# Kernel optimization log

Measured on AMD Instinct MI355X. Metric: run time of the kernel, lower is better.

The kernel has to match this reference:

```python
import math
import jax, jax.numpy as jnp
import numpy as np

B, S, D, H = 2, 2048, 2048, 16
HD = D // H
EPS = 1e-6


def _precompute_freqs_cis(dim, end, theta=500000.0):
    inv_freqs = 1.0 / theta ** (np.arange(0, dim, 2, dtype=np.float32) / dim)
    t = np.arange(end, dtype=np.float32)
    freqs = np.outer(t, inv_freqs).astype(np.float32)
    # [1, end, 1, dim//2, 2] matching torch stack(cos, sin, dim=4)
    return jnp.asarray(np.stack([np.cos(freqs)[None, :, None, :], np.sin(freqs)[None, :, None, :]], axis=4))


def setup_inputs() -> dict:
    key = jax.random.key(0)
    k1, k2, k3 = jax.random.split(key, 3)
    x = jax.random.normal(k1, (B, S, D), dtype=jnp.float32)
    w_qkv = jax.random.normal(k2, (3 * D, D), dtype=jnp.float32) * 0.02
    w_out = jax.random.normal(k3, (D, D), dtype=jnp.float32) * 0.02
    attn_scale = jnp.asarray(math.log2(S * S - S), dtype=jnp.float32)
    freqs_cis = _precompute_freqs_cis(HD, S)
    return {"x": x, "w_qkv": w_qkv, "w_out": w_out, "attn_scale": attn_scale, "freqs_cis": freqs_cis}


def _apply_rotary(q, k, fc):
    # q, k: [b, s, h, hd]; fc: [1, s, 1, hd//2, 2]
    b, s, h, hd = q.shape
    qk = jnp.concatenate([q, k], axis=2).reshape(b, s, 2 * h, hd // 2, 2)
    real = qk[..., 0] * fc[..., 0] - qk[..., 1] * fc[..., 1]
    imag = qk[..., 1] * fc[..., 0] + qk[..., 0] * fc[..., 1]
    rot = jnp.stack([real, imag], axis=-1).reshape(b, s, 2 * h, hd)
    return rot[:, :, :h], rot[:, :, h:]


def reference(x, w_qkv, w_out, attn_scale, freqs_cis):
    b, s, d = x.shape
    qkv = x @ w_qkv.T                      # [b, s, 3d]
    q, k, v = jnp.split(qkv, 3, axis=2)
    q = q.reshape(b, s, H, HD)
    k = k.reshape(b, s, H, HD)
    v = v.reshape(b, s, H, HD)
    q, k = _apply_rotary(q, k, freqs_cis[:, :s])
    # -> [b, h, s, hd]
    q = q.transpose(0, 2, 1, 3)
    k = k.transpose(0, 2, 1, 3)
    v = v.transpose(0, 2, 1, 3)
    # per-head L2 norm of q/k, learned scale on q
    q = q / (jnp.linalg.norm(q, axis=-1, keepdims=True) + EPS)
    k = k / (jnp.linalg.norm(k, axis=-1, keepdims=True) + EPS)
    q = q * attn_scale
    # causal SDPA with scale=1.0
    scores = jnp.einsum('bhqd,bhkd->bhqk', q, k)
    causal = jnp.tril(jnp.ones((s, s), dtype=bool))
    scores = jnp.where(causal, scores, -jnp.inf)
    attn = jax.nn.softmax(scores, axis=-1)
    out = jnp.einsum('bhqk,bhkd->bhqd', attn, v)
    out = out.transpose(0, 2, 1, 3).reshape(b, s, d)
    return out @ w_out.T
```

## Files before the change

### kernel.cpp

```cpp
#include <hip/hip_runtime.h>
#include <stdint.h>

#define B_  2
#define S_  2048
#define D_  2048
#define H_  16
#define HD_ 128
#define D3_ 6144

typedef unsigned short u16;
typedef __attribute__((ext_vector_type(8))) __bf16 bf16x8;
typedef __attribute__((ext_vector_type(4))) float f32x4;
typedef __attribute__((ext_vector_type(8))) u16  u16x8;
typedef __attribute__((ext_vector_type(4))) u16  u16x4;
typedef __attribute__((ext_vector_type(2))) u16  u16x2;

__device__ inline u16 f2bf(float f) {
  union { float f; uint32_t u; } v; v.f = f;
  uint32_t r = v.u + 0x7FFFu + ((v.u >> 16) & 1u);
  return (u16)(r >> 16);
}
__device__ inline float bf2f(u16 u) {
  union { float f; uint32_t u; } v; v.u = ((uint32_t)u) << 16;
  return v.f;
}
__device__ inline void gload_lds16(const void* g, void* l) {
  __builtin_amdgcn_global_load_lds((const __attribute__((address_space(1))) uint32_t*)g,
                                   (__attribute__((address_space(3))) uint32_t*)l, 16, 0, 0);
}

#define TILE_SYNC() do { \
    asm volatile("s_waitcnt lgkmcnt(0)" ::: "memory"); \
    asm volatile("s_waitcnt vmcnt(0)" ::: "memory"); \
    __builtin_amdgcn_s_barrier(); \
    asm volatile("" ::: "memory"); \
  } while (0)

__global__ __launch_bounds__(256) void castk3(const float* __restrict__ x, const float* __restrict__ wq,
                                              const float* __restrict__ wo,
                                              u16* __restrict__ xo, u16* __restrict__ wqo, u16* __restrict__ woo) {
  int blk = (int)blockIdx.x;
  const float* in; u16* out; int base;
  if (blk < 4096)       { in = x;  out = xo;  base = blk; }
  else if (blk < 10240) { in = wq; out = wqo; base = blk - 4096; }
  else                  { in = wo; out = woo; base = blk - 10240; }
  int i = base * 256 + (int)threadIdx.x;
  f32x4 a = ((const f32x4*)in)[2*i];
  f32x4 b = ((const f32x4*)in)[2*i + 1];
  u16x8 o;
#pragma unroll
  for (int j = 0; j < 4; ++j) o[j] = f2bf(a[j]);
#pragma unroll
  for (int j = 0; j < 4; ++j) o[4+j] = f2bf(b[j]);
  ((u16x8*)out)[i] = o;
}

template<int BF16OUT>
__global__ __launch_bounds__(512, 2) void gemm384(const u16* __restrict__ A, const u16* __restrict__ Bw,
                                                  void* __restrict__ Cp, int M, int N, int K) {
  __shared__ __align__(16) u16 lds_[40960];
  char* ldsb = (char*)lds_;
  const int tid = threadIdx.x;
  const int w = tid >> 6, l = tid & 63;
  const int lr = l & 15, lg = l >> 4;
  const int wr = w >> 2, wc = w & 3;
  const int nbn = (int)gridDim.x;
  const int nwg = nbn * (int)gridDim.y;
  const int bid = (int)(blockIdx.y * gridDim.x + blockIdx.x);
  const int swz = (bid & 7) * (nwg >> 3) + (bid >> 3);
  const int bm = swz / nbn, bn = swz % nbn;

  f32x4 acc[8][6] = {};

  int mA[2], kA[2], mB[3], kB[3];
#pragma unroll
  for (int p = 0; p < 2; ++p) {
    int off = p*8192 + tid*16; mA[p] = off >> 6;
    kA[p] = (off & 63) ^ (((mA[p] >> 1) & 3) << 4);
  }
#pragma unroll
  for (int p = 0; p < 3; ++p) {
    int off = p*8192 + tid*16; mB[p] = off >> 6;
    kB[p] = (off & 63) ^ (((mB[p] >> 1) & 3) << 4);
  }
  const size_t rs = (size_t)K * 2;
  const char* Ab = (const char*)A + (size_t)bm * 256 * rs;
  const char* Bb = (const char*)Bw + (size_t)bn * 384 * rs;
  const int wb = w * 1024;

#define STG(T_) do { \
    char* dA_ = ldsb + ((T_)&1)*16384; \
    char* dB_ = ldsb + 32768 + ((T_)&1)*24576; \
    _Pragma("unroll") \
    for (int p_ = 0; p_ < 2; ++p_) \
      gload_lds16(Ab + (size_t)mA[p_]*rs + (size_t)(T_)*64 + kA[p_], dA_ + p_*8192 + wb); \
    _Pragma("unroll") \
    for (int p_ = 0; p_ < 3; ++p_) \
      gload_lds16(Bb + (size_t)mB[p_]*rs + (size_t)(T_)*64 + kB[p_], dB_ + p_*8192 + wb); \
  } while (0)

  const int NT = K >> 5;
  STG(0);
  TILE_SYNC();

  for (int T = 0; T < NT; ++T) {
    const char* La = ldsb + (T & 1)*16384;
    const char* Lb = ldsb + 32768 + (T & 1)*24576;
    if (T + 1 < NT) STG(T + 1);

    bf16x8 bfr[6];
#pragma unroll
    for (int nf = 0; nf < 6; ++nf) {
      int row = wc*96 + nf*16 + lr;
      bfr[nf] = *(const bf16x8*)(Lb + row*64 + ((lg*16) ^ (((row >> 1) & 3) << 4)));
    }
#pragma unroll
    for (int mf = 0; mf < 8; ++mf) {
      int row = wr*128 + mf*16 + lr;
      bf16x8 af = *(const bf16x8*)(La + row*64 + ((lg*16) ^ (((row >> 1) & 3) << 4)));
#pragma unroll
      for (int nf = 0; nf < 6; ++nf)
        acc[mf][nf] = __builtin_amdgcn_mfma_f32_16x16x32_bf16(af, bfr[nf], acc[mf][nf], 0, 0, 0);
    }
    TILE_SYNC();
  }
#undef STG

#pragma unroll
  for (int mf = 0; mf < 8; ++mf)
#pragma unroll
    for (int nf = 0; nf < 6; ++nf)
#pragma unroll
      for (int j = 0; j < 4; ++j) {
        int m = bm*256 + wr*128 + mf*16 + lg*4 + j;
        int n = bn*384 + wc*96 + nf*16 + lr;
        float v = acc[mf][nf][j];
        if (BF16OUT) ((u16*)Cp)[(size_t)m * N + n] = f2bf(v);
        else         ((float*)Cp)[(size_t)m * N + n] = v;
      }
}

template<int BF16OUT>
__global__ __launch_bounds__(256, 2) void gemm_bt(const u16* __restrict__ A, const u16* __restrict__ Bw,
                                                  void* __restrict__ Cp, int M, int N, int K) {
  __shared__ __align__(16) u16 lds_[32768];
  char* ldsb = (char*)lds_;
  const int tid = threadIdx.x;
  const int w = tid >> 6, l = tid & 63;
  const int lr = l & 15, lg = l >> 4;
  const int nwg = (int)(gridDim.x * gridDim.y);
  const int bid = (int)(blockIdx.y * gridDim.x + blockIdx.x);
  const int swz = (bid & 7) * (nwg >> 3) + (bid >> 3);
  const int bm = swz / (int)gridDim.x, bn = swz % (int)gridDim.x;
  const int wr = w >> 1, wc = w & 1;

  f32x4 acc[4][4] = {};

  int row4[4], col4[4];
#pragma unroll
  for (int i = 0; i < 4; ++i) {
    int off = i*4096 + tid*16;
    row4[i] = off >> 7;
    col4[i] = (off & 127) ^ ((row4[i] & 7) << 4);
  }
  const size_t rs = (size_t)K * 2;
  const char* Ab = (const char*)A + (size_t)bm * 128 * rs;
  const char* Bb = (const char*)Bw + (size_t)bn * 128 * rs;
  const int wb = w * 1024;

#define STG(T_) do { \
    char* dA_ = ldsb + ((T_)&1)*16384; \
    char* dB_ = ldsb + 32768 + ((T_)&1)*16384; \
    _Pragma("unroll") \
    for (int i_ = 0; i_ < 4; ++i_) \
      gload_lds16(Ab + (size_t)row4[i_]*rs + (size_t)(T_)*128 + col4[i_], dA_ + i_*4096 + wb); \
    _Pragma("unroll") \
    for (int i_ = 0; i_ < 4; ++i_) \
      gload_lds16(Bb + (size_t)row4[i_]*rs + (size_t)(T_)*128 + col4[i_], dB_ + i_*4096 + wb); \
  } while (0)

  const int NT = K >> 6;
  STG(0);
  TILE_SYNC();

  for (int T = 0; T < NT; ++T) {
    const char* La = ldsb + (T & 1)*16384;
    const char* Lb = ldsb + 32768 + (T & 1)*16384;
    if (T + 1 < NT) STG(T + 1);

    bf16x8 af[4][2], bf[4][2];
#pragma unroll
    for (int mt = 0; mt < 4; ++mt) {
      int row = wr*64 + mt*16 + lr;
#pragma unroll
      for (int ks = 0; ks < 2; ++ks)
        af[mt][ks] = *(const bf16x8*)(La + row*128 + ((ks*64 + lg*16) ^ ((row & 7) << 4)));
    }
#pragma unroll
    for (int nt = 0; nt < 4; ++nt) {
      int row = wc*64 + nt*16 + lr;
#pragma unroll
      for (int ks = 0; ks < 2; ++ks)
        bf[nt][ks] = *(const bf16x8*)(Lb + row*128 + ((ks*64 + lg*16) ^ ((row & 7) << 4)));
    }
#pragma unroll
    for (int mt = 0; mt < 4; ++mt)
#pragma unroll
      for (int nt = 0; nt < 4; ++nt) {
        acc[mt][nt] = __builtin_amdgcn_mfma_f32_16x16x32_bf16(af[mt][0], bf[nt][0], acc[mt][nt], 0, 0, 0);
        acc[mt][nt] = __builtin_amdgcn_mfma_f32_16x16x32_bf16(af[mt][1], bf[nt][1], acc[mt][nt], 0, 0, 0);
      }
    TILE_SYNC();
  }
#undef STG

#pragma unroll
  for (int mt = 0; mt < 4; ++mt)
#pragma unroll
    for (int nt = 0; nt < 4; ++nt)
#pragma unroll
      for (int j = 0; j < 4; ++j) {
        int m = bm*128 + wr*64 + mt*16 + lg*4 + j;
        int n = bn*128 + wc*64 + nt*16 + lr;
        float v = acc[mt][nt][j];
        if (BF16OUT) ((u16*)Cp)[(size_t)m * N + n] = f2bf(v);
        else         ((float*)Cp)[(size_t)m * N + n] = v;
      }
}

__global__ __launch_bounds__(256) void rope_norm(const u16* __restrict__ qkv, const float* __restrict__ fc,
                                                 const float* __restrict__ scale_p,
                                                 u16* __restrict__ Qo, u16* __restrict__ Ko) {
  int gid = blockIdx.x;
  int bs = gid >> 2;
  int s = bs & (S_ - 1);
  int b = bs >> 11;
  int w = threadIdx.x >> 6, l = threadIdx.x & 63;
  int h = (gid & 3)*4 + w;
  float2 cs = ((const float2*)fc)[(size_t)s*64 + l];
  float scale = scale_p[0] * 1.4426950408889634f;
  const u16* base = qkv + (size_t)bs * D3_;
  size_t obase = ((size_t)(b*H_ + h) * S_ + s) * HD_ + 2*l;
  {
    const u16* p = base + h*HD_ + 2*l;
    float x0 = bf2f(p[0]), x1 = bf2f(p[1]);
    float r0 = x0*cs.x - x1*cs.y;
    float r1 = x1*cs.x + x0*cs.y;
    float t = r0*r0 + r1*r1;
#pragma unroll
    for (int mk = 1; mk < 64; mk <<= 1) t += __shfl_xor(t, mk, 64);
    float inv = scale / (sqrtf(t) + 1e-6f);
    u16x2 o; o[0] = f2bf(r0*inv); o[1] = f2bf(r1*inv);
    *(u16x2*)(Qo + obase) = o;
  }
  {
    const u16* p = base + D_ + h*HD_ + 2*l;
    float x0 = bf2f(p[0]), x1 = bf2f(p[1]);
    float r0 = x0*cs.x - x1*cs.y;
    float r1 = x1*cs.x + x0*cs.y;
    float t = r0*r0 + r1*r1;
#pragma unroll
    for (int mk = 1; mk < 64; mk <<= 1) t += __shfl_xor(t, mk, 64);
    float inv = 1.0f / (sqrtf(t) + 1e-6f);
    u16x2 o; o[0] = f2bf(r0*inv); o[1] = f2bf(r1*inv);
    *(u16x2*)(Ko + obase) = o;
  }
}

__global__ __launch_bounds__(256) void v_trans(const u16* __restrict__ qkv, u16* __restrict__ Vt) {
  __shared__ u16 vt[64][136];
  int blk = blockIdx.x;
  int bh = blk >> 5, st = blk & 31;
  int b = bh >> 4, h = bh & 15;
  int s0 = st * 64;
  int tid = threadIdx.x;
#pragma unroll
  for (int i = 0; i < 4; ++i) {
    int idx = tid + i*256;
    int row = idx >> 4, ch = idx & 15;
    u16x8 v = *(const u16x8*)(qkv + (size_t)(b*S_ + s0 + row) * D3_ + 2*D_ + h*HD_ + ch*8);
    *(u16x8*)(&vt[row][ch*8]) = v;
  }
  __syncthreads();
#pragma unroll
  for (int p = 0; p < 2; ++p) {
    int d = p*64 + (tid >> 2);
    int q = (tid & 3) * 16;
    u16x8 t0, t1;
#pragma unroll
    for (int i = 0; i < 8; ++i) t0[i] = vt[q + i][d];
#pragma unroll
    for (int i = 0; i < 8; ++i) t1[i] = vt[q + 8 + i][d];
    u16* dst = Vt + ((size_t)bh * HD_ + d) * S_ + s0 + q;
    *(u16x8*)dst = t0;
    *(u16x8*)(dst + 8) = t1;
  }
}

__global__ __launch_bounds__(512) void flash_attn(const u16* __restrict__ Qh, const u16* __restrict__ Kh,
                                                  const u16* __restrict__ Vt, u16* __restrict__ AO) {
  __shared__ __align__(16) u16 lK[2][64*128];
  __shared__ __align__(16) u16 lV[128*64];
  __shared__ __align__(16) u16 lP[8][16*72];
  const int i0 = (int)blockIdx.x;
  const int k5 = i0 & 255;
  const int bh = k5 >> 3;
  const int jj = k5 & 7;
  const int qt = (i0 < 256) ? (15 - jj) : jj;
  const int tid = threadIdx.x, w = tid >> 6, l = tid & 63;
  const int lr = l & 15, lg = l >> 4;
  const int b = bh >> 4, h = bh & 15;

  bf16x8 qf[4];
  {
    const u16* qp = Qh + ((size_t)bh * S_ + qt*128 + w*16 + lr) * HD_ + lg*8;
#pragma unroll
    for (int ks = 0; ks < 4; ++ks) qf[ks] = *(const bf16x8*)(qp + ks*32);
  }
  float m0 = -__builtin_inff(), ls0 = 0.f;
  f32x4 oacc[8] = {};

  int krow[2], kcol[2], vrow[2], vcol[2], dstb[2];
#pragma unroll
  for (int p = 0; p < 2; ++p) {
    int off = p*8192 + tid*16;
    krow[p] = off >> 8; kcol[p] = (off & 255) ^ ((krow[p] & 7) << 4);
    vrow[p] = off >> 7; vcol[p] = (off & 127) ^ ((vrow[p] & 7) << 4);
    dstb[p] = p*8192 + w*1024;
  }
  const char* Kb = (const char*)(Kh + (size_t)bh * S_ * HD_);
  const char* Vb = (const char*)(Vt + (size_t)bh * HD_ * S_);

#define STAGE_K(nb, kt_) do {                                                       \
    _Pragma("unroll")                                                               \
    for (int p_ = 0; p_ < 2; ++p_)                                                  \
      gload_lds16(Kb + (size_t)((kt_)*64 + krow[p_])*256 + kcol[p_],                \
                  (char*)lK[nb] + dstb[p_]);                                        \
  } while (0)
#define STAGE_V(kt_) do {                                                           \
    _Pragma("unroll")                                                               \
    for (int p_ = 0; p_ < 2; ++p_)                                                  \
      gload_lds16(Vb + (size_t)vrow[p_]*(S_*2) + (kt_)*128 + vcol[p_],              \
                  (char*)lV + dstb[p_]);                                            \
  } while (0)

  const int nt = 2*qt + 2;
  STAGE_K(0, 0);
  STAGE_V(0);
  int cur = 0;
  for (int kt = 0; kt < nt; ++kt) {
    asm volatile("s_waitcnt vmcnt(2)" ::: "memory");
    __builtin_amdgcn_s_barrier();
    asm volatile("" ::: "memory");
    const char* lKb = (const char*)lK[cur];

    f32x4 sc[4] = {};
    __builtin_amdgcn_s_setprio(1);
#pragma unroll
    for (int ks = 0; ks < 4; ++ks) {
#pragma unroll
      for (int f = 0; f < 4; ++f) {
        int row = f*16 + lr;
        bf16x8 kf = *(const bf16x8*)(lKb + row*256 + ((ks*64 + lg*16) ^ ((row & 7) << 4)));
        sc[f] = __builtin_amdgcn_mfma_f32_16x16x32_bf16(kf, qf[ks], sc[f], 0, 0, 0);
      }
    }
    __builtin_amdgcn_s_setprio(0);
    if (kt < nt-1) STAGE_K(cur ^ 1, kt + 1);

    if (kt >= nt-2) {
#pragma unroll
      for (int f = 0; f < 4; ++f)
#pragma unroll
        for (int j = 0; j < 4; ++j)
          if (kt*64 + f*16 + lg*4 + j > qt*128 + w*16 + lr) sc[f][j] = -__builtin_inff();
    }
    float pmax = sc[0][0];
#pragma unroll
    for (int f = 0; f < 4; ++f)
#pragma unroll
      for (int j = 0; j < 4; ++j) pmax = fmaxf(pmax, sc[f][j]);
    pmax = fmaxf(pmax, __shfl_xor(pmax, 16, 64));
    pmax = fmaxf(pmax, __shfl_xor(pmax, 32, 64));
    const int norescale = __all(pmax - m0 <= 8.0f);
    float mn;
    float resc = 0.f;
    if (norescale) {
      mn = m0;
    } else {
      mn = fmaxf(m0, pmax);
      resc = exp2f(m0 - mn);
      m0 = mn;
    }
    float rsum = 0.f;
#pragma unroll
    for (int f = 0; f < 4; ++f)
#pragma unroll
      for (int j = 0; j < 4; ++j) {
        float p = exp2f(sc[f][j] - mn);
        sc[f][j] = p;
        rsum += p;
      }
    rsum += __shfl_xor(rsum, 16, 64);
    rsum += __shfl_xor(rsum, 32, 64);
    if (norescale) {
      ls0 = ls0 + rsum;
    } else {
      ls0 = ls0 * resc + rsum;
      float rescj[4];
#pragma unroll
      for (int j = 0; j < 4; ++j) rescj[j] = __shfl(resc, lg*4 + j, 64);
#pragma unroll
      for (int fd = 0; fd < 8; ++fd)
#pragma unroll
        for (int j = 0; j < 4; ++j) oacc[fd][j] *= rescj[j];
    }
#pragma unroll
    for (int f = 0; f < 4; ++f) {
      u16x4 pk;
#pragma unroll
      for (int j = 0; j < 4; ++j) pk[j] = f2bf(sc[f][j]);
      *(u16x4*)((char*)lP[w] + lr*144 + f*32 + lg*8) = pk;
    }

    if (kt < nt-1) { asm volatile("s_waitcnt vmcnt(2)" ::: "memory"); }
    else           { asm volatile("s_waitcnt vmcnt(0)" ::: "memory"); }
    __builtin_amdgcn_s_barrier();
    asm volatile("" ::: "memory");
    __builtin_amdgcn_s_setprio(1);
#pragma unroll
    for (int ks = 0; ks < 2; ++ks) {
      bf16x8 pf = *(const bf16x8*)((const char*)lP[w] + lr*144 + ks*64 + lg*16);
#pragma unroll
      for (int fd = 0; fd < 8; ++fd) {
        int row = fd*16 + lr;
        bf16x8 vf = *(const bf16x8*)((const char*)lV + row*128 + ((ks*64 + lg*16) ^ ((row & 7) << 4)));
        oacc[fd] = __builtin_amdgcn_mfma_f32_16x16x32_bf16(pf, vf, oacc[fd], 0, 0, 0);
      }
    }
    __builtin_amdgcn_s_setprio(0);
    asm volatile("" ::: "memory");
    __builtin_amdgcn_s_barrier();
    asm volatile("" ::: "memory");
    if (kt < nt-1) STAGE_V(kt + 1);
    cur ^= 1;
  }
#undef STAGE_K
#undef STAGE_V
  float invl[4];
#pragma unroll
  for (int j = 0; j < 4; ++j) {
    float lsj = __shfl(ls0, lg*4 + j, 64);
    invl[j] = 1.0f / lsj;
  }
#pragma unroll
  for (int fd = 0; fd < 8; ++fd)
#pragma unroll
    for (int j = 0; j < 4; ++j) {
      int qq = qt*128 + w*16 + lg*4 + j;
      int dd = fd*16 + lr;
      float v = oacc[fd][j] * invl[j];
      AO[((size_t)b*S_ + qq)*D_ + h*HD_ + dd] = f2bf(v);
    }
}

extern "C" void kernel_launch(void* const* d_in, const int* in_sizes, int n_in,
                              void* d_out, int out_size, void* d_ws, size_t ws_size,
                              hipStream_t stream) {
  const float* x        = (const float*)d_in[0];
  const float* w_qkv    = (const float*)d_in[1];
  const float* w_out    = (const float*)d_in[2];
  const float* attn_sc  = (const float*)d_in[3];
  const float* freqs    = (const float*)d_in[4];

  if (ws_size < 167772160u) return;

  char* ws = (char*)d_ws;
  u16* xbf  = (u16*)(ws);
  u16* wqbf = (u16*)(ws + 16777216);
  u16* wobf = (u16*)(ws + 41943040);
  u16* qkv  = (u16*)(ws + 50331648);
  u16* Qh   = (u16*)(ws + 100663296);
  u16* Kh   = (u16*)(ws + 117440512);
  u16* Vt   = (u16*)(ws + 134217728);
  u16* AO   = (u16*)(ws + 150994944);

  castk3<<<12288, 256, 0, stream>>>(x, w_qkv, w_out, xbf, wqbf, wobf);

  gemm384<1><<<dim3(16, 16), 512, 0, stream>>>(xbf, wqbf, qkv, 4096, 6144, 2048);

  rope_norm<<<16384, 256, 0, stream>>>(qkv, freqs, attn_sc, Qh, Kh);
  v_trans<<<1024, 256, 0, stream>>>(qkv, Vt);

  flash_attn<<<512, 512, 0, stream>>>(Qh, Kh, Vt, AO);

  gemm_bt<0><<<dim3(16, 32), 256, 0, stream>>>(AO, wobf, (float*)d_out, 4096, 2048, 2048);
}
```

Before: 250.2 us.

## Halve output GEMM K-tile for three-block occupancy and merge rope/V-transpose kernels

The output-projection GEMM now stages K-tiles of 32 instead of 64. This halves LDS use so three workgroups can fit per CU, and the LDS swizzle is adjusted to the 64-byte row stride. Separately, the rope/norm kernel and the V-transpose kernel are merged into one launch by splitting on block index, which removes one launch and its tail gap. In exchange the GEMM runs twice as many K iterations with a barrier each, so sync overhead rises. The merged kernel also reserves LDS in every block, which may lower rope-block occupancy.

```diff
diff --git a/kernel.cpp b/kernel.cpp
--- a/kernel.cpp
+++ b/kernel.cpp
@@ -141,9 +141,9 @@
 }
 
 template<int BF16OUT>
-__global__ __launch_bounds__(256, 2) void gemm_bt(const u16* __restrict__ A, const u16* __restrict__ Bw,
-                                                  void* __restrict__ Cp, int M, int N, int K) {
-  __shared__ __align__(16) u16 lds_[32768];
+__global__ __launch_bounds__(256, 3) void gemm_o(const u16* __restrict__ A, const u16* __restrict__ Bw,
+                                                 void* __restrict__ Cp, int M, int N, int K) {
+  __shared__ __align__(16) u16 lds_[16384];
   char* ldsb = (char*)lds_;
   const int tid = threadIdx.x;
   const int w = tid >> 6, l = tid & 63;
@@ -156,12 +156,12 @@
 
   f32x4 acc[4][4] = {};
 
-  int row4[4], col4[4];
-#pragma unroll
-  for (int i = 0; i < 4; ++i) {
-    int off = i*4096 + tid*16;
-    row4[i] = off >> 7;
-    col4[i] = (off & 127) ^ ((row4[i] & 7) << 4);
+  int m2[2], k2[2];
+#pragma unroll
+  for (int p = 0; p < 2; ++p) {
+    int off = p*4096 + tid*16;
+    m2[p] = off >> 6;
+    k2[p] = (off & 63) ^ (((m2[p] >> 1) & 3) << 4);
   }
   const size_t rs = (size_t)K * 2;
   const char* Ab = (const char*)A + (size_t)bm * 128 * rs;
@@ -169,47 +169,40 @@
   const int wb = w * 1024;
 
 #define STG(T_) do { \
-    char* dA_ = ldsb + ((T_)&1)*16384; \
-    char* dB_ = ldsb + 32768 + ((T_)&1)*16384; \
+    char* dA_ = ldsb + ((T_)&1)*8192; \
+    char* dB_ = ldsb + 16384 + ((T_)&1)*8192; \
     _Pragma("unroll") \
-    for (int i_ = 0; i_ < 4; ++i_) \
-      gload_lds16(Ab + (size_t)row4[i_]*rs + (size_t)(T_)*128 + col4[i_], dA_ + i_*4096 + wb); \
-    _Pragma("unroll") \
-    for (int i_ = 0; i_ < 4; ++i_) \
-      gload_lds16(Bb + (size_t)row4[i_]*rs + (size_t)(T_)*128 + col4[i_], dB_ + i_*4096 + wb); \
+    for (int p_ = 0; p_ < 2; ++p_) { \
+      gload_lds16(Ab + (size_t)m2[p_]*rs + (size_t)(T_)*64 + k2[p_], dA_ + p_*4096 + wb); \
+      gload_lds16(Bb + (size_t)m2[p_]*rs + (size_t)(T_)*64 + k2[p_], dB_ + p_*4096 + wb); \
+    } \
   } while (0)
 
-  const int NT = K >> 6;
+  const int NT = K >> 5;
   STG(0);
   TILE_SYNC();
 
   for (int T = 0; T < NT; ++T) {
-    const char* La = ldsb + (T & 1)*16384;
-    const char* Lb = ldsb + 32768 + (T & 1)*16384;
+    const char* La = ldsb + (T & 1)*8192;
+    const char* Lb = ldsb + 16384 + (T & 1)*8192;
     if (T + 1 < NT) STG(T + 1);
 
-    bf16x8 af[4][2], bf[4][2];
+    bf16x8 af[4], bf[4];
 #pragma unroll
     for (int mt = 0; mt < 4; ++mt) {
       int row = wr*64 + mt*16 + lr;
-#pragma unroll
-      for (int ks = 0; ks < 2; ++ks)
-        af[mt][ks] = *(const bf16x8*)(La + row*128 + ((ks*64 + lg*16) ^ ((row & 7) << 4)));
+      af[mt] = *(const bf16x8*)(La + row*64 + ((lg*16) ^ (((row >> 1) & 3) << 4)));
     }
 #pragma unroll
     for (int nt = 0; nt < 4; ++nt) {
       int row = wc*64 + nt*16 + lr;
-#pragma unroll
-      for (int ks = 0; ks < 2; ++ks)
-        bf[nt][ks] = *(const bf16x8*)(Lb + row*128 + ((ks*64 + lg*16) ^ ((row & 7) << 4)));
+      bf[nt] = *(const bf16x8*)(Lb + row*64 + ((lg*16) ^ (((row >> 1) & 3) << 4)));
     }
 #pragma unroll
     for (int mt = 0; mt < 4; ++mt)
 #pragma unroll
-      for (int nt = 0; nt < 4; ++nt) {
-        acc[mt][nt] = __builtin_amdgcn_mfma_f32_16x16x32_bf16(af[mt][0], bf[nt][0], acc[mt][nt], 0, 0, 0);
-        acc[mt][nt] = __builtin_amdgcn_mfma_f32_16x16x32_bf16(af[mt][1], bf[nt][1], acc[mt][nt], 0, 0, 0);
-      }
+      for (int nt = 0; nt < 4; ++nt)
+        acc[mt][nt] = __builtin_amdgcn_mfma_f32_16x16x32_bf16(af[mt], bf[nt], acc[mt][nt], 0, 0, 0);
     TILE_SYNC();
   }
 #undef STG
@@ -228,72 +221,73 @@
       }
 }
 
-__global__ __launch_bounds__(256) void rope_norm(const u16* __restrict__ qkv, const float* __restrict__ fc,
-                                                 const float* __restrict__ scale_p,
-                                                 u16* __restrict__ Qo, u16* __restrict__ Ko) {
-  int gid = blockIdx.x;
-  int bs = gid >> 2;
-  int s = bs & (S_ - 1);
-  int b = bs >> 11;
-  int w = threadIdx.x >> 6, l = threadIdx.x & 63;
-  int h = (gid & 3)*4 + w;
-  float2 cs = ((const float2*)fc)[(size_t)s*64 + l];
-  float scale = scale_p[0] * 1.4426950408889634f;
-  const u16* base = qkv + (size_t)bs * D3_;
-  size_t obase = ((size_t)(b*H_ + h) * S_ + s) * HD_ + 2*l;
-  {
-    const u16* p = base + h*HD_ + 2*l;
-    float x0 = bf2f(p[0]), x1 = bf2f(p[1]);
-    float r0 = x0*cs.x - x1*cs.y;
-    float r1 = x1*cs.x + x0*cs.y;
-    float t = r0*r0 + r1*r1;
-#pragma unroll
-    for (int mk = 1; mk < 64; mk <<= 1) t += __shfl_xor(t, mk, 64);
-    float inv = scale / (sqrtf(t) + 1e-6f);
-    u16x2 o; o[0] = f2bf(r0*inv); o[1] = f2bf(r1*inv);
-    *(u16x2*)(Qo + obase) = o;
-  }
-  {
-    const u16* p = base + D_ + h*HD_ + 2*l;
-    float x0 = bf2f(p[0]), x1 = bf2f(p[1]);
-    float r0 = x0*cs.x - x1*cs.y;
-    float r1 = x1*cs.x + x0*cs.y;
-    float t = r0*r0 + r1*r1;
-#pragma unroll
-    for (int mk = 1; mk < 64; mk <<= 1) t += __shfl_xor(t, mk, 64);
-    float inv = 1.0f / (sqrtf(t) + 1e-6f);
-    u16x2 o; o[0] = f2bf(r0*inv); o[1] = f2bf(r1*inv);
-    *(u16x2*)(Ko + obase) = o;
-  }
-}
-
-__global__ __launch_bounds__(256) void v_trans(const u16* __restrict__ qkv, u16* __restrict__ Vt) {
-  __shared__ u16 vt[64][136];
-  int blk = blockIdx.x;
-  int bh = blk >> 5, st = blk & 31;
-  int b = bh >> 4, h = bh & 15;
-  int s0 = st * 64;
-  int tid = threadIdx.x;
-#pragma unroll
-  for (int i = 0; i < 4; ++i) {
-    int idx = tid + i*256;
-    int row = idx >> 4, ch = idx & 15;
-    u16x8 v = *(const u16x8*)(qkv + (size_t)(b*S_ + s0 + row) * D3_ + 2*D_ + h*HD_ + ch*8);
-    *(u16x8*)(&vt[row][ch*8]) = v;
-  }
-  __syncthreads();
-#pragma unroll
-  for (int p = 0; p < 2; ++p) {
-    int d = p*64 + (tid >> 2);
-    int q = (tid & 3) * 16;
-    u16x8 t0, t1;
-#pragma unroll
-    for (int i = 0; i < 8; ++i) t0[i] = vt[q + i][d];
-#pragma unroll
-    for (int i = 0; i < 8; ++i) t1[i] = vt[q + 8 + i][d];
-    u16* dst = Vt + ((size_t)bh * HD_ + d) * S_ + s0 + q;
-    *(u16x8*)dst = t0;
-    *(u16x8*)(dst + 8) = t1;
+__global__ __launch_bounds__(256) void rope_vt(const u16* __restrict__ qkv, const float* __restrict__ fc,
+                                               const float* __restrict__ scale_p,
+                                               u16* __restrict__ Qo, u16* __restrict__ Ko,
+                                               u16* __restrict__ Vt) {
+  int gid = (int)blockIdx.x;
+  if (gid < 16384) {
+    int bs = gid >> 2;
+    int s = bs & (S_ - 1);
+    int b = bs >> 11;
+    int w = threadIdx.x >> 6, l = threadIdx.x & 63;
+    int h = (gid & 3)*4 + w;
+    float2 cs = ((const float2*)fc)[(size_t)s*64 + l];
+    float scale = scale_p[0] * 1.4426950408889634f;
+    const u16* base = qkv + (size_t)bs * D3_;
+    size_t obase = ((size_t)(b*H_ + h) * S_ + s) * HD_ + 2*l;
+    {
+      const u16* p = base + h*HD_ + 2*l;
+      float x0 = bf2f(p[0]), x1 = bf2f(p[1]);
+      float r0 = x0*cs.x - x1*cs.y;
+      float r1 = x1*cs.x + x0*cs.y;
+      float t = r0*r0 + r1*r1;
+#pragma unroll
+      for (int mk = 1; mk < 64; mk <<= 1) t += __shfl_xor(t, mk, 64);
+      float inv = scale / (sqrtf(t) + 1e-6f);
+      u16x2 o; o[0] = f2bf(r0*inv); o[1] = f2bf(r1*inv);
+      *(u16x2*)(Qo + obase) = o;
+    }
+    {
+      const u16* p = base + D_ + h*HD_ + 2*l;
+      float x0 = bf2f(p[0]), x1 = bf2f(p[1]);
+      float r0 = x0*cs.x - x1*cs.y;
+      float r1 = x1*cs.x + x0*cs.y;
+      float t = r0*r0 + r1*r1;
+#pragma unroll
+      for (int mk = 1; mk < 64; mk <<= 1) t += __shfl_xor(t, mk, 64);
+      float inv = 1.0f / (sqrtf(t) + 1e-6f);
+      u16x2 o; o[0] = f2bf(r0*inv); o[1] = f2bf(r1*inv);
+      *(u16x2*)(Ko + obase) = o;
+    }
+  } else {
+    __shared__ u16 vt[64][136];
+    int blk = gid - 16384;
+    int bh = blk >> 5, st = blk & 31;
+    int b = bh >> 4, h = bh & 15;
+    int s0 = st * 64;
+    int tid = threadIdx.x;
+#pragma unroll
+    for (int i = 0; i < 4; ++i) {
+      int idx = tid + i*256;
+      int row = idx >> 4, ch = idx & 15;
+      u16x8 v = *(const u16x8*)(qkv + (size_t)(b*S_ + s0 + row) * D3_ + 2*D_ + h*HD_ + ch*8);
+      *(u16x8*)(&vt[row][ch*8]) = v;
+    }
+    __syncthreads();
+#pragma unroll
+    for (int p = 0; p < 2; ++p) {
+      int d = p*64 + (tid >> 2);
+      int q = (tid & 3) * 16;
+      u16x8 t0, t1;
+#pragma unroll
+      for (int i = 0; i < 8; ++i) t0[i] = vt[q + i][d];
+#pragma unroll
+      for (int i = 0; i < 8; ++i) t1[i] = vt[q + 8 + i][d];
+      u16* dst = Vt + ((size_t)bh * HD_ + d) * S_ + s0 + q;
+      *(u16x8*)dst = t0;
+      *(u16x8*)(dst + 8) = t1;
+    }
   }
 }
 
@@ -489,10 +483,9 @@
 
   gemm384<1><<<dim3(16, 16), 512, 0, stream>>>(xbf, wqbf, qkv, 4096, 6144, 2048);
 
-  rope_norm<<<16384, 256, 0, stream>>>(qkv, freqs, attn_sc, Qh, Kh);
-  v_trans<<<1024, 256, 0, stream>>>(qkv, Vt);
+  rope_vt<<<17408, 256, 0, stream>>>(qkv, freqs, attn_sc, Qh, Kh, Vt);
 
   flash_attn<<<512, 512, 0, stream>>>(Qh, Kh, Vt, AO);
 
-  gemm_bt<0><<<dim3(16, 32), 256, 0, stream>>>(AO, wobf, (float*)d_out, 4096, 2048, 2048);
-}
+  gemm_o<0><<<dim3(16, 32), 256, 0, stream>>>(AO, wobf, (float*)d_out, 4096, 2048, 2048);
+}
```

Result: slower. 256.6 us (+2.5%).
